# Kernel optimization log

Measured on AMD Instinct MI355X. Metric: run time of the kernel, lower is better.

## Reference

```python
import math
import jax, jax.numpy as jnp
import numpy as np

B, S, D = 8, 1024, 1024
H, DK = 16, 64
NUM_BUCKETS, MAX_DIST = 32, 128
LN_EPS = 1e-6


def _relative_position_bucket(relative_position, num_buckets=NUM_BUCKETS, max_distance=MAX_DIST):
    # bidirectional (encoder) variant of T5 bucketing
    nb = num_buckets // 2
    rel_buckets = (relative_position > 0).astype(jnp.int32) * nb
    rp = jnp.abs(relative_position)
    max_exact = nb // 2
    is_small = rp < max_exact
    rp_large = max_exact + (
        jnp.log(jnp.maximum(rp, 1).astype(jnp.float32) / max_exact)
        / math.log(max_distance / max_exact)
        * (nb - max_exact)
    ).astype(jnp.int32)
    rp_large = jnp.minimum(rp_large, nb - 1)
    return rel_buckets + jnp.where(is_small, rp, rp_large)


def compute_bias(rel_bias, q_len, k_len):
    ctx = jnp.arange(q_len)[:, None]
    mem = jnp.arange(k_len)[None, :]
    buckets = _relative_position_bucket(mem - ctx)        # [q,k]
    values = rel_bias[buckets]                             # [q,k,H]
    return jnp.transpose(values, (2, 0, 1))[None]          # [1,H,q,k]


def switch_layer_norm(x, w, eps=LN_EPS):
    # T5-style: no mean subtraction, no bias
    var = jnp.mean(jnp.square(x.astype(jnp.float32)), axis=-1, keepdims=True)
    return w * (x * jax.lax.rsqrt(var + eps)).astype(x.dtype)


def setup_inputs() -> dict:
    key = jax.random.key(0)
    ks = jax.random.split(key, 6)
    scale = 1.0 / math.sqrt(D)
    return {
        "hidden_states": jax.random.normal(ks[0], (B, S, D), jnp.float32),
        "ln_weight": jnp.ones((D,), jnp.float32),
        "wq": jax.random.normal(ks[1], (D, H * DK), jnp.float32) * scale,
        "wk": jax.random.normal(ks[2], (D, H * DK), jnp.float32) * scale,
        "wv": jax.random.normal(ks[3], (D, H * DK), jnp.float32) * scale,
        "wo": jax.random.normal(ks[4], (H * DK, D), jnp.float32) * scale,
        "rel_bias": jax.random.normal(ks[5], (NUM_BUCKETS, H), jnp.float32),
    }


def reference(hidden_states, ln_weight, wq, wk, wv, wo, rel_bias):
    b, s, d = hidden_states.shape
    normed = switch_layer_norm(hidden_states, ln_weight)
    # projections -> [B,H,S,DK]; T5 applies NO 1/sqrt(dk) scaling
    q = (normed @ wq).reshape(b, s, H, DK).transpose(0, 2, 1, 3)
    k = (normed @ wk).reshape(b, s, H, DK).transpose(0, 2, 1, 3)
    v = (normed @ wv).reshape(b, s, H, DK).transpose(0, 2, 1, 3)
    scores = jnp.einsum("bhqd,bhkd->bhqk", q, k)
    scores = scores + compute_bias(rel_bias, s, s)
    attn = jax.nn.softmax(scores, axis=-1)
    ctx = jnp.einsum("bhqk,bhkd->bhqd", attn, v)
    ctx = ctx.transpose(0, 2, 1, 3).reshape(b, s, H * DK)
    attn_out = ctx @ wo
    return hidden_states + attn_out  # residual of SwitchLayerSelfAttention (dropout=0)
```

## Files before the change

kernel.cpp:

```cpp
#include <hip/hip_runtime.h>

typedef unsigned short u16;
typedef unsigned int u32;
typedef unsigned long long u64;
typedef __attribute__((ext_vector_type(8))) short bf16x8;
typedef __attribute__((ext_vector_type(4))) float f32x4;

__device__ __forceinline__ float bf2f(u16 u) {
  union { u32 i; float f; } c; c.i = ((u32)u) << 16; return c.f;
}
__device__ __forceinline__ u16 f2bf(float f) {
  union { float f; u32 i; } c; c.f = f;
  u32 i = c.i;
  return (u16)((i + 0x7fffu + ((i >> 16) & 1u)) >> 16);
}
__device__ __forceinline__ u32 pkbf(float a, float b) {
  union { float f; u32 i; } ca, cb; ca.f = a; cb.f = b;
  return __builtin_amdgcn_perm(cb.i + 0x8000u, ca.i + 0x8000u, 0x07060302u);
}
__device__ __forceinline__ void async16(const void* g, void* l) {
  __builtin_amdgcn_global_load_lds((const __attribute__((address_space(1))) void*)g,
                                   (__attribute__((address_space(3))) void*)l, 16, 0, 0);
}

__global__ __launch_bounds__(256) void detect_kernel(const u32* __restrict__ X,
                                                     int* __restrict__ flag) {
  __shared__ int part[4];
  const int tid = threadIdx.x, lane = tid & 63, wave = tid >> 6;
  int votes = 0;
  for (int i = tid; i < 4096; i += 256) {
    const u32 u = X[i];
    union { u32 i; float f; } c; c.i = u;
    const float a = fabsf(c.f);
    if (u == 0u || (a > 1e-6f && a < 1e6f)) votes++;
  }
  #pragma unroll
  for (int off = 32; off >= 1; off >>= 1) votes += __shfl_xor(votes, off);
  if (lane == 0) part[wave] = votes;
  __syncthreads();
  if (tid == 0) {
    const int tot = part[0] + part[1] + part[2] + part[3];
    *flag = (tot >= 2048) ? 0 : 1;
  }
}

__global__ __launch_bounds__(256) void prep_rms_kernel(
    const void* __restrict__ W0, const void* __restrict__ W1, const void* __restrict__ W2,
    const void* __restrict__ W3, u16* __restrict__ T0, u16* __restrict__ T1,
    u16* __restrict__ T2, u16* __restrict__ T3, const void* __restrict__ rel_bias,
    float* __restrict__ Tb, const void* __restrict__ X, const void* __restrict__ LnW,
    u16* __restrict__ Normed, const int* __restrict__ flagp) {
  const int f32m = (*flagp == 0);
  const int z = blockIdx.z;
  if (z >= 5) {
    __shared__ float part[4];
    const int tid = threadIdx.x, lane = tid & 63, wave = tid >> 6;
    const size_t row = (size_t)(z - 5) * 256 + blockIdx.y * 16 + blockIdx.x;
    const int c = tid * 4;
    float x0, x1, x2, x3, w0f, w1f, w2f, w3f;
    if (f32m) {
      const float4 xx = *(const float4*)((const float*)X + row * 1024 + c);
      x0 = xx.x; x1 = xx.y; x2 = xx.z; x3 = xx.w;
      const float4 ww = *(const float4*)((const float*)LnW + c);
      w0f = ww.x; w1f = ww.y; w2f = ww.z; w3f = ww.w;
    } else {
      const u32* px = (const u32*)((const u16*)X + row * 1024 + c);
      const u32 a0 = px[0], a1 = px[1];
      x0 = bf2f((u16)a0); x1 = bf2f((u16)(a0 >> 16));
      x2 = bf2f((u16)a1); x3 = bf2f((u16)(a1 >> 16));
      const u32* pw = (const u32*)((const u16*)LnW + c);
      const u32 b0 = pw[0], b1 = pw[1];
      w0f = bf2f((u16)b0); w1f = bf2f((u16)(b0 >> 16));
      w2f = bf2f((u16)b1); w3f = bf2f((u16)(b1 >> 16));
    }
    float ss = x0 * x0 + x1 * x1 + x2 * x2 + x3 * x3;
    #pragma unroll
    for (int off = 32; off >= 1; off >>= 1) ss += __shfl_xor(ss, off);
    if (lane == 0) part[wave] = ss;
    __syncthreads();
    const float tot = part[0] + part[1] + part[2] + part[3];
    const float scale = rsqrtf(tot * (1.0f / 1024.0f) + 1e-6f);
    const u16 o0 = f2bf(x0 * scale * w0f);
    const u16 o1 = f2bf(x1 * scale * w1f);
    const u16 o2 = f2bf(x2 * scale * w2f);
    const u16 o3 = f2bf(x3 * scale * w3f);
    u32* po = (u32*)(Normed + row * 1024 + c);
    po[0] = (u32)o0 | ((u32)o1 << 16);
    po[1] = (u32)o2 | ((u32)o3 << 16);
    return;
  }
  if (z == 4) {
    const int flat = blockIdx.y * 16 + blockIdx.x;
    const int idx = flat * 256 + threadIdx.x;
    if (idx >= 16 * 2047) return;
    const int h = idx / 2047;
    const int d = idx % 2047 - 1023;
    const int rb = (d > 0) ? 16 : 0;
    const int rp = d < 0 ? -d : d;
    int val;
    if (rp < 8) {
      val = rp;
    } else {
      float t = (logf((float)rp * 0.125f) / 2.772588722239781f) * 8.0f;
      val = 8 + (int)t;
      if (val > 15) val = 15;
    }
    const int bi = (rb + val) * 16 + h;
    Tb[idx] = f32m ? ((const float*)rel_bias)[bi] : bf2f(((const u16*)rel_bias)[bi]);
    return;
  }
  const void* W = (z == 0) ? W0 : (z == 1) ? W1 : (z == 2) ? W2 : W3;
  u16* WT = (z == 0) ? T0 : (z == 1) ? T1 : (z == 2) ? T2 : T3;
  __shared__ u16 t[64][65];
  const int tid = threadIdx.x;
  const int tx = tid & 63, ty = tid >> 6;
  const int n0 = blockIdx.x * 64, k0 = blockIdx.y * 64;
  #pragma unroll
  for (int r = ty; r < 64; r += 4) {
    const size_t idx = (size_t)(k0 + r) * 1024 + n0 + tx;
    t[r][tx] = f32m ? f2bf(((const float*)W)[idx]) : ((const u16*)W)[idx];
  }
  __syncthreads();
  #pragma unroll
  for (int r = ty; r < 64; r += 4) WT[(size_t)(n0 + r) * 1024 + k0 + tx] = t[tx][r];
}

template <int S0>
__device__ __forceinline__ void stage3(u16* lds, const u16* __restrict__ A,
                                       const u16* __restrict__ B, int m0, int n0,
                                       int kt, int w, int lane) {
  const int ko8 = ((lane & 7) ^ ((lane >> 3) & 7)) * 8;
  const int rl = lane >> 3;
  #pragma unroll
  for (int s = S0; s < S0 + 3; ++s) {
    const int cw = s * 8 + w;
    const int r = cw * 8 + rl;
    u16* ldst = lds + cw * 512;
    if (s < 4)
      async16(A + (size_t)(m0 + r) * 1024 + kt + ko8, ldst);
    else
      async16(B + (size_t)(n0 + r - 256) * 1024 + kt + ko8, ldst);
  }
}

template <bool SWAP>
__device__ __forceinline__ void gemm256_core(const u16* __restrict__ A,
                                             const u16* __restrict__ WT,
                                             u16 (*buf)[24576], f32x4 (&acc)[4][4],
                                             int m0, int n0, int lane, int w) {
  const int wr = w >> 1, wc = w & 1;
  const int l15 = lane & 15;
  const int ko0 = (((lane >> 4) + 0) ^ (lane & 7)) * 8;
  const int ko1 = (((lane >> 4) + 4) ^ (lane & 7)) * 8;
  const int arow = (wr * 64 + l15) * 64;
  const int brow = 16384 + (wc * 64 + l15) * 64;

  stage3<0>(buf[0], A, WT, m0, n0, 0, w, lane);
  stage3<3>(buf[0], A, WT, m0, n0, 0, w, lane);
  stage3<0>(buf[1], A, WT, m0, n0, 64, w, lane);
  stage3<3>(buf[1], A, WT, m0, n0, 64, w, lane);
  __asm__ volatile("s_waitcnt vmcnt(6)" ::: "memory");
  __builtin_amdgcn_s_barrier();
  __asm__ volatile("" ::: "memory");

  int sl = 0, sn = 2;
  #pragma unroll 1
  for (int t = 0; t < 16; ++t) {
    const u16* bc = buf[sl];
    u16* bn = buf[sn];
    const int kt2 = (t + 2) * 64;
    bf16x8 af[4][2], bfr[2][2];
    #pragma unroll
    for (int i = 0; i < 4; ++i) {
      af[i][0] = *(const bf16x8*)(bc + arow + i * 1024 + ko0);
      af[i][1] = *(const bf16x8*)(bc + arow + i * 1024 + ko1);
    }
    #pragma unroll
    for (int j = 0; j < 2; ++j) {
      bfr[j][0] = *(const bf16x8*)(bc + brow + j * 1024 + ko0);
      bfr[j][1] = *(const bf16x8*)(bc + brow + j * 1024 + ko1);
    }
    if (t < 14) stage3<0>(bn, A, WT, m0, n0, kt2, w, lane);
    __builtin_amdgcn_s_barrier();
    __asm__ volatile("s_waitcnt lgkmcnt(0)" ::: "memory");
    __builtin_amdgcn_s_setprio(1);
    #pragma unroll
    for (int i = 0; i < 4; ++i)
      #pragma unroll
      for (int j = 0; j < 2; ++j) {
        if (SWAP) {
          acc[i][j] = __builtin_amdgcn_mfma_f32_16x16x32_bf16(bfr[j][0], af[i][0], acc[i][j], 0, 0, 0);
          acc[i][j] = __builtin_amdgcn_mfma_f32_16x16x32_bf16(bfr[j][1], af[i][1], acc[i][j], 0, 0, 0);
        } else {
          acc[i][j] = __builtin_amdgcn_mfma_f32_16x16x32_bf16(af[i][0], bfr[j][0], acc[i][j], 0, 0, 0);
          acc[i][j] = __builtin_amdgcn_mfma_f32_16x16x32_bf16(af[i][1], bfr[j][1], acc[i][j], 0, 0, 0);
        }
      }
    __builtin_amdgcn_s_setprio(0);
    __builtin_amdgcn_s_barrier();
    __asm__ volatile("" ::: "memory");
    #pragma unroll
    for (int j = 0; j < 2; ++j) {
      bfr[j][0] = *(const bf16x8*)(bc + brow + (j + 2) * 1024 + ko0);
      bfr[j][1] = *(const bf16x8*)(bc + brow + (j + 2) * 1024 + ko1);
    }
    if (t < 14) stage3<3>(bn, A, WT, m0, n0, kt2, w, lane);
    __builtin_amdgcn_s_barrier();
    __asm__ volatile("s_waitcnt lgkmcnt(0)" ::: "memory");
    __builtin_amdgcn_s_setprio(1);
    #pragma unroll
    for (int i = 0; i < 4; ++i)
      #pragma unroll
      for (int j = 0; j < 2; ++j) {
        if (SWAP) {
          acc[i][j + 2] = __builtin_amdgcn_mfma_f32_16x16x32_bf16(bfr[j][0], af[i][0], acc[i][j + 2], 0, 0, 0);
          acc[i][j + 2] = __builtin_amdgcn_mfma_f32_16x16x32_bf16(bfr[j][1], af[i][1], acc[i][j + 2], 0, 0, 0);
        } else {
          acc[i][j + 2] = __builtin_amdgcn_mfma_f32_16x16x32_bf16(af[i][0], bfr[j][0], acc[i][j + 2], 0, 0, 0);
          acc[i][j + 2] = __builtin_amdgcn_mfma_f32_16x16x32_bf16(af[i][1], bfr[j][1], acc[i][j + 2], 0, 0, 0);
        }
      }
    __builtin_amdgcn_s_setprio(0);
    if (t < 14)
      __asm__ volatile("s_waitcnt vmcnt(6)" ::: "memory");
    else
      __asm__ volatile("s_waitcnt vmcnt(0)" ::: "memory");
    __builtin_amdgcn_s_barrier();
    __asm__ volatile("" ::: "memory");
    sl = (sl == 2) ? 0 : sl + 1;
    sn = (sn == 2) ? 0 : sn + 1;
  }
}

__device__ __forceinline__ void stageK32(u16* lds, const u16* __restrict__ A,
                                         const u16* __restrict__ B, int m0, int n0,
                                         int kt, int w, int lane) {
  const int sp = (lane & 7) ^ ((lane >> 3) & 7);
  const int rl = 2 * (lane >> 3) + (sp >> 2);
  const int ko = (sp & 3) * 8;
  #pragma unroll
  for (int s = 0; s < 3; ++s) {
    const int cw = s * 8 + w;
    u16* ldst = lds + cw * 512;
    if (s < 2)
      async16(A + (size_t)(m0 + cw * 16 + rl) * 1024 + kt + ko, ldst);
    else
      async16(B + (size_t)(n0 + (cw - 16) * 16 + rl) * 1024 + kt + ko, ldst);
  }
}

template <bool SWAP>
__device__ __forceinline__ void gemmK32_core(const u16* __restrict__ A,
                                             const u16* __restrict__ WT,
                                             u16 (*buf)[12288], f32x4 (&acc)[4][4],
                                             int m0, int n0, int lane, int w) {
  const int wr = w >> 1, wc = w & 1;
  const int l15 = lane & 15, quad = lane >> 4;
  const int sw = ((quad + 4 * (lane & 1)) ^ ((l15 >> 1) & 7)) * 8;
  const int abase = (wr * 32 + (l15 >> 1)) * 64 + sw;
  const int bbase = 8192 + (wc * 32 + (l15 >> 1)) * 64 + sw;

  stageK32(buf[0], A, WT, m0, n0, 0, w, lane);
  stageK32(buf[1], A, WT, m0, n0, 32, w, lane);
  __asm__ volatile("s_waitcnt vmcnt(3)" ::: "memory");
  __builtin_amdgcn_s_barrier();
  __asm__ volatile("" ::: "memory");

  int sl = 0, sn = 2;
  #pragma unroll 1
  for (int t = 0; t < 32; ++t) {
    const u16* bc = buf[sl];
    bf16x8 af[4], bfr[4];
    #pragma unroll
    for (int i = 0; i < 4; ++i) af[i] = *(const bf16x8*)(bc + abase + i * 512);
    #pragma unroll
    for (int j = 0; j < 4; ++j) bfr[j] = *(const bf16x8*)(bc + bbase + j * 512);
    if (t < 30) stageK32(buf[sn], A, WT, m0, n0, (t + 2) * 32, w, lane);
    __asm__ volatile("s_waitcnt lgkmcnt(0)" ::: "memory");
    __builtin_amdgcn_s_setprio(1);
    #pragma unroll
    for (int i = 0; i < 4; ++i)
      #pragma unroll
      for (int j = 0; j < 4; ++j) {
        if (SWAP)
          acc[i][j] = __builtin_amdgcn_mfma_f32_16x16x32_bf16(bfr[j], af[i], acc[i][j], 0, 0, 0);
        else
          acc[i][j] = __builtin_amdgcn_mfma_f32_16x16x32_bf16(af[i], bfr[j], acc[i][j], 0, 0, 0);
      }
    __builtin_amdgcn_s_setprio(0);
    if (t < 30)
      __asm__ volatile("s_waitcnt vmcnt(3)" ::: "memory");
    else
      __asm__ volatile("s_waitcnt vmcnt(0)" ::: "memory");
    __builtin_amdgcn_s_barrier();
    __asm__ volatile("" ::: "memory");
    sl = (sl == 2) ? 0 : sl + 1;
    sn = (sn == 2) ? 0 : sn + 1;
  }
}

__global__ __launch_bounds__(512, 4) void qkv_gemm32_kernel(
    const u16* __restrict__ A, const u16* __restrict__ WT,
    u16* __restrict__ Qo, u16* __restrict__ Ko, u16* __restrict__ VTo) {
  __shared__ __align__(16) u16 buf[3][12288];
  const int tid = threadIdx.x, lane = tid & 63, w = tid >> 6;
  const int id = blockIdx.x;
  const int xcd = id & 7;
  const int t0 = id >> 3;
  const int nb = t0 % 24;
  const int mhi = t0 / 24;
  const int m0 = (mhi * 8 + xcd) * 256;
  const int n0 = nb * 128;
  const int z = nb >> 3;

  f32x4 acc[4][4];
  const f32x4 zero = {0.f, 0.f, 0.f, 0.f};
  #pragma unroll
  for (int i = 0; i < 4; ++i)
    #pragma unroll
    for (int j = 0; j < 4; ++j) acc[i][j] = zero;

  const int wr = w >> 1, wc = w & 1;
  const int cq = lane & 15, quad = lane >> 4;
  const int nbase = (n0 & 1023) + wc * 64;

  if (z == 2) {
    gemmK32_core<false>(A, WT, buf, acc, m0, n0, lane, w);
    #pragma unroll
    for (int i = 0; i < 4; ++i) {
      const int s = m0 + wr * 64 + i * 16 + quad * 4;
      const int b = s >> 10, s0 = s & 1023;
      #pragma unroll
      for (int j = 0; j < 4; ++j) {
        const int n = nbase + j * 16 + cq;
        const int hh = n >> 6, dk = n & 63;
        const u64 pk = (u64)f2bf(acc[i][j][0]) | ((u64)f2bf(acc[i][j][1]) << 16) |
                       ((u64)f2bf(acc[i][j][2]) << 32) | ((u64)f2bf(acc[i][j][3]) << 48);
        *(u64*)(VTo + (((size_t)(b * 16 + hh)) * 64 + dk) * 1024 + s0) = pk;
      }
    }
  } else {
    gemmK32_core<true>(A, WT, buf, acc, m0, n0, lane, w);
    u16* Out = (z == 0) ? Qo : Ko;
    #pragma unroll
    for (int i = 0; i < 4; ++i) {
      const int s = m0 + wr * 64 + i * 16 + cq;
      const int b = s >> 10, ss = s & 1023;
      #pragma unroll
      for (int j = 0; j < 4; ++j) {
        const int n = nbase + j * 16 + quad * 4;
        const int hh = n >> 6, dk = n & 63;
        const u64 pk = (u64)f2bf(acc[i][j][0]) | ((u64)f2bf(acc[i][j][1]) << 16) |
                       ((u64)f2bf(acc[i][j][2]) << 32) | ((u64)f2bf(acc[i][j][3]) << 48);
        *(u64*)(Out + (((size_t)(b * 16 + hh)) * 1024 + ss) * 64 + dk) = pk;
      }
    }
  }
}

__global__ __launch_bounds__(512, 2) void out_gemm256_kernel(
    const u16* __restrict__ A, const u16* __restrict__ BT, const void* __restrict__ Res,
    void* __restrict__ Out, const int* __restrict__ flagp) {
  const int f32m = (*flagp == 0);
  __shared__ __align__(16) u16 buf[3][24576];
  const int tid = threadIdx.x, lane = tid & 63, w = tid >> 6;
  const int id = blockIdx.x;
  const int xcd = id & 7;
  const int t0 = id >> 3;
  const int nb = t0 & 7;
  const int mhi = t0 >> 3;
  const int m0 = (mhi * 8 + xcd) * 256;
  const int n0 = nb * 128;

  f32x4 acc[4][4];
  const f32x4 zero = {0.f, 0.f, 0.f, 0.f};
  #pragma unroll
  for (int i = 0; i < 4; ++i)
    #pragma unroll
    for (int j = 0; j < 4; ++j) acc[i][j] = zero;

  gemm256_core<true>(A, BT, buf, acc, m0, n0, lane, w);

  const int wr = w >> 1, wc = w & 1;
  const int cq = lane & 15, quad = lane >> 4;
  #pragma unroll
  for (int i = 0; i < 4; ++i) {
    const int s = m0 + wr * 64 + i * 16 + cq;
    #pragma unroll
    for (int j = 0; j < 4; ++j) {
      const int n = n0 + wc * 64 + j * 16 + quad * 4;
      const size_t idx = (size_t)s * 1024 + n;
      if (f32m) {
        const float4 rr = *(const float4*)((const float*)Res + idx);
        float4 oo;
        oo.x = rr.x + acc[i][j][0]; oo.y = rr.y + acc[i][j][1];
        oo.z = rr.z + acc[i][j][2]; oo.w = rr.w + acc[i][j][3];
        *(float4*)((float*)Out + idx) = oo;
      } else {
        const u64 rr = *(const u64*)((const u16*)Res + idx);
        const u64 pk =
            (u64)f2bf(bf2f((u16)rr) + acc[i][j][0]) |
            ((u64)f2bf(bf2f((u16)(rr >> 16)) + acc[i][j][1]) << 16) |
            ((u64)f2bf(bf2f((u16)(rr >> 32)) + acc[i][j][2]) << 32) |
            ((u64)f2bf(bf2f((u16)(rr >> 48)) + acc[i][j][3]) << 48);
        *(u64*)((u16*)Out + idx) = pk;
      }
    }
  }
}

__global__ __launch_bounds__(512, 4) void attn_kernel(
    const u16* __restrict__ Q, const u16* __restrict__ K, const u16* __restrict__ VT,
    const float* __restrict__ Tb, u16* __restrict__ ctx) {
  __shared__ __align__(16) u16 Ks[3][4096];
  __shared__ __align__(16) u16 Vs[2][4096];
  __shared__ __align__(16) u16 Ps[8][2048];
  __shared__ __align__(16) float Tbs[1280];

  const int tid = threadIdx.x, lane = tid & 63, w = tid >> 6;
  const int c = lane & 15, quad = lane >> 4;
  const int id = blockIdx.x;
  const int bh = id & 127, qc = id >> 7;
  const int b = bh >> 4, h = bh & 15;
  const int q0 = qc * 256;
  const int qw = q0 + w * 32;
  const u16* Kg = K + (size_t)bh * 1024 * 64;
  const u16* Vg = VT + (size_t)bh * 64 * 1024;
  const float* Th = Tb + h * 2047;
  u16* PsW = &Ps[w][0];

  for (int i = tid; i < 1280; i += 512) Tbs[i] = Th[768 - q0 + i];

  bf16x8 qf[2][2];
  {
    const u16* Qg = Q + ((size_t)bh * 1024 + qw) * 64;
    #pragma unroll
    for (int nt = 0; nt < 2; ++nt)
      #pragma unroll
      for (int half = 0; half < 2; ++half)
        qf[nt][half] = *(const bf16x8*)(Qg + (size_t)(nt * 16 + c) * 64 + half * 32 + quad * 8);
  }

  f32x4 oacc[4][2];
  const f32x4 zero = {0.f, 0.f, 0.f, 0.f};
  #pragma unroll
  for (int i = 0; i < 4; ++i)
    #pragma unroll
    for (int j = 0; j < 2; ++j) oacc[i][j] = zero;
  float rsum[2] = {0.f, 0.f};

  const u16* Ksrc = Kg + (size_t)((w >> 1) * 16 + c) * 64 + (w & 1) * 32 + quad * 8;
  const u16* Vsrc = Vg + (size_t)((w >> 1) * 16 + c) * 1024 + (w & 1) * 32 + quad * 8;

  async16(Vsrc, &Vs[0][w * 512]);
  async16(Ksrc, &Ks[0][w * 512]);
  async16(Ksrc + (size_t)64 * 64, &Ks[1][w * 512]);
  __asm__ volatile("s_waitcnt lgkmcnt(0)" ::: "memory");

  int sl = 0, sn = 2;
  #pragma unroll 1
  for (int kt = 0; kt < 16; ++kt) {
    const int k0 = kt * 64;
    const u16* Kc = &Ks[sl][0];
    const u16* Vc = &Vs[kt & 1][0];
    if (kt < 15)
      __asm__ volatile("s_waitcnt vmcnt(1)" ::: "memory");
    else
      __asm__ volatile("s_waitcnt vmcnt(0)" ::: "memory");
    __builtin_amdgcn_s_barrier();
    __asm__ volatile("" ::: "memory");
    if (kt < 15) async16(Vsrc + (kt + 1) * 64, &Vs[(kt + 1) & 1][w * 512]);
    if (kt < 14) async16(Ksrc + (size_t)((kt + 2) * 64) * 64, &Ks[sn][w * 512]);
    f32x4 sc[4][2];
    const int jb = k0 + quad * 4 - c + 255 - 32 * w;
    #pragma unroll
    for (int mt = 0; mt < 4; ++mt)
      #pragma unroll
      for (int nt = 0; nt < 2; ++nt) {
        const float* tp = Tbs + jb + mt * 16 - nt * 16;
        sc[mt][nt][0] = tp[0]; sc[mt][nt][1] = tp[1]; sc[mt][nt][2] = tp[2]; sc[mt][nt][3] = tp[3];
      }
    __builtin_amdgcn_s_setprio(1);
    #pragma unroll
    for (int mt = 0; mt < 4; ++mt) {
      const bf16x8 kf0 = *(const bf16x8*)(Kc + (mt * 2 + 0) * 512 + lane * 8);
      const bf16x8 kf1 = *(const bf16x8*)(Kc + (mt * 2 + 1) * 512 + lane * 8);
      #pragma unroll
      for (int nt = 0; nt < 2; ++nt) {
        sc[mt][nt] = __builtin_amdgcn_mfma_f32_16x16x32_bf16(kf0, qf[nt][0], sc[mt][nt], 0, 0, 0);
        sc[mt][nt] = __builtin_amdgcn_mfma_f32_16x16x32_bf16(kf1, qf[nt][1], sc[mt][nt], 0, 0, 0);
      }
    }
    __builtin_amdgcn_s_setprio(0);
    #pragma unroll
    for (int mt = 0; mt < 4; ++mt)
      #pragma unroll
      for (int nt = 0; nt < 2; ++nt) {
        const float p0 = __expf(sc[mt][nt][0]), p1 = __expf(sc[mt][nt][1]);
        const float p2 = __expf(sc[mt][nt][2]), p3 = __expf(sc[mt][nt][3]);
        rsum[nt] += (p0 + p1) + (p2 + p3);
        const u32 lo = pkbf(p0, p1), hi = pkbf(p2, p3);
        const u64 pk = (u64)lo | ((u64)hi << 32);
        const int ch = (mt * 2 + (quad >> 1)) ^ (c & 7);
        *(u64*)(PsW + (nt * 16 + c) * 64 + ch * 8 + (quad & 1) * 4) = pk;
      }
    __asm__ volatile("s_waitcnt lgkmcnt(0)" ::: "memory");
    bf16x8 pf[2][2];
    #pragma unroll
    for (int nt = 0; nt < 2; ++nt)
      #pragma unroll
      for (int kk = 0; kk < 2; ++kk) {
        const int ch = (kk * 4 + quad) ^ (c & 7);
        pf[nt][kk] = *(const bf16x8*)(PsW + (nt * 16 + c) * 64 + ch * 8);
      }
    __builtin_amdgcn_s_setprio(1);
    #pragma unroll
    for (int dt = 0; dt < 4; ++dt) {
      const bf16x8 vf0 = *(const bf16x8*)(Vc + (dt * 2 + 0) * 512 + lane * 8);
      const bf16x8 vf1 = *(const bf16x8*)(Vc + (dt * 2 + 1) * 512 + lane * 8);
      #pragma unroll
      for (int nt = 0; nt < 2; ++nt) {
        oacc[dt][nt] = __builtin_amdgcn_mfma_f32_16x16x32_bf16(vf0, pf[nt][0], oacc[dt][nt], 0, 0, 0);
        oacc[dt][nt] = __builtin_amdgcn_mfma_f32_16x16x32_bf16(vf1, pf[nt][1], oacc[dt][nt], 0, 0, 0);
      }
    }
    __builtin_amdgcn_s_setprio(0);
    sl = (sl == 2) ? 0 : sl + 1;
    sn = (sn == 2) ? 0 : sn + 1;
  }

  #pragma unroll
  for (int nt = 0; nt < 2; ++nt) {
    rsum[nt] += __shfl_xor(rsum[nt], 16);
    rsum[nt] += __shfl_xor(rsum[nt], 32);
  }

  #pragma unroll
  for (int nt = 0; nt < 2; ++nt) {
    const float inv = 1.0f / rsum[nt];
    const int q = qw + nt * 16 + c;
    #pragma unroll
    for (int dt = 0; dt < 4; ++dt) {
      const u64 pk = (u64)f2bf(oacc[dt][nt][0] * inv) | ((u64)f2bf(oacc[dt][nt][1] * inv) << 16) |
                     ((u64)f2bf(oacc[dt][nt][2] * inv) << 32) | ((u64)f2bf(oacc[dt][nt][3] * inv) << 48);
      *(u64*)(ctx + (((size_t)b * 1024 + q) * 16 + h) * 64 + dt * 16 + quad * 4) = pk;
    }
  }
}

extern "C" void kernel_launch(void* const* d_in, const int* in_sizes, int n_in,
                              void* d_out, int out_size, void* d_ws, size_t ws_size,
                              hipStream_t stream) {
  const void* hidden = d_in[0];
  const void* lnw = d_in[1];
  const void* wq = d_in[2];
  const void* wk = d_in[3];
  const void* wv = d_in[4];
  const void* wo = d_in[5];
  const void* relb = d_in[6];
  char* ws = (char*)d_ws;

  u16* normed = (u16*)(ws);
  u16* Qb = (u16*)(ws + ((size_t)16 << 20));
  u16* Kb = (u16*)(ws + ((size_t)32 << 20));
  u16* VTb = (u16*)(ws + ((size_t)48 << 20));
  u16* wtq = (u16*)(ws + ((size_t)64 << 20));
  u16* wtk = (u16*)(ws + ((size_t)64 << 20) + (2 << 20));
  u16* wtv = (u16*)(ws + ((size_t)64 << 20) + (4 << 20));
  u16* wto = (u16*)(ws + ((size_t)64 << 20) + (6 << 20));
  float* Tb = (float*)(ws + ((size_t)64 << 20) + (8 << 20));
  int* flag = (int*)(ws + ((size_t)64 << 20) + (9 << 20));

  dim3 b256(256);
  detect_kernel<<<dim3(1), b256, 0, stream>>>((const u32*)hidden, flag);
  prep_rms_kernel<<<dim3(16, 16, 37), b256, 0, stream>>>(wq, wk, wv, wo, wtq, wtk, wtv,
                                                         wto, relb, Tb, hidden, lnw,
                                                         normed, flag);
  qkv_gemm32_kernel<<<dim3(768), dim3(512), 0, stream>>>(normed, wtq, Qb, Kb, VTb);
  attn_kernel<<<dim3(512), dim3(512), 0, stream>>>(Qb, Kb, VTb, Tb, normed);
  out_gemm256_kernel<<<dim3(256), dim3(512), 0, stream>>>(normed, wto, hidden, d_out, flag);
}
```

Baseline: 244.7 us.

## Fold dtype detection into kernels and switch output GEMM to K32 core

Removes the separate single-block detect kernel launch and its flag buffer. Each block of the prep and output-projection kernels now recomputes the input-dtype vote itself. The output projection also moves from the 256-deep-K pipelined core to the K32 core used by the QKV GEMM, with half the LDS and a launch bound of 4 blocks per CU for better occupancy. The cost is redundant 16KB reads plus a block barrier in every one of the roughly nine thousand prep blocks and in every output block.

```diff
diff --git a/kernel.cpp b/kernel.cpp
--- a/kernel.cpp
+++ b/kernel.cpp
@@ -23,12 +23,12 @@
                                    (__attribute__((address_space(3))) void*)l, 16, 0, 0);
 }
 
-__global__ __launch_bounds__(256) void detect_kernel(const u32* __restrict__ X,
-                                                     int* __restrict__ flag) {
-  __shared__ int part[4];
-  const int tid = threadIdx.x, lane = tid & 63, wave = tid >> 6;
+template <int NT>
+__device__ __forceinline__ int detect_f32(const u32* __restrict__ X, int* part,
+                                          int tid, int lane, int wave) {
   int votes = 0;
-  for (int i = tid; i < 4096; i += 256) {
+  #pragma unroll
+  for (int i = tid; i < 4096; i += NT) {
     const u32 u = X[i];
     union { u32 i; float f; } c; c.i = u;
     const float a = fabsf(c.f);
@@ -38,10 +38,10 @@
   for (int off = 32; off >= 1; off >>= 1) votes += __shfl_xor(votes, off);
   if (lane == 0) part[wave] = votes;
   __syncthreads();
-  if (tid == 0) {
-    const int tot = part[0] + part[1] + part[2] + part[3];
-    *flag = (tot >= 2048) ? 0 : 1;
-  }
+  int tot = 0;
+  #pragma unroll
+  for (int i = 0; i < NT / 64; ++i) tot += part[i];
+  return (tot >= 2048) ? 1 : 0;
 }
 
 __global__ __launch_bounds__(256) void prep_rms_kernel(
@@ -49,8 +49,10 @@
     const void* __restrict__ W3, u16* __restrict__ T0, u16* __restrict__ T1,
     u16* __restrict__ T2, u16* __restrict__ T3, const void* __restrict__ rel_bias,
     float* __restrict__ Tb, const void* __restrict__ X, const void* __restrict__ LnW,
-    u16* __restrict__ Normed, const int* __restrict__ flagp) {
-  const int f32m = (*flagp == 0);
+    u16* __restrict__ Normed) {
+  __shared__ int dpart[4];
+  const int tid0 = threadIdx.x;
+  const int f32m = detect_f32<256>((const u32*)X, dpart, tid0, tid0 & 63, tid0 >> 6);
   const int z = blockIdx.z;
   if (z >= 5) {
     __shared__ float part[4];
@@ -125,113 +127,6 @@
   for (int r = ty; r < 64; r += 4) WT[(size_t)(n0 + r) * 1024 + k0 + tx] = t[tx][r];
 }
 
-template <int S0>
-__device__ __forceinline__ void stage3(u16* lds, const u16* __restrict__ A,
-                                       const u16* __restrict__ B, int m0, int n0,
-                                       int kt, int w, int lane) {
-  const int ko8 = ((lane & 7) ^ ((lane >> 3) & 7)) * 8;
-  const int rl = lane >> 3;
-  #pragma unroll
-  for (int s = S0; s < S0 + 3; ++s) {
-    const int cw = s * 8 + w;
-    const int r = cw * 8 + rl;
-    u16* ldst = lds + cw * 512;
-    if (s < 4)
-      async16(A + (size_t)(m0 + r) * 1024 + kt + ko8, ldst);
-    else
-      async16(B + (size_t)(n0 + r - 256) * 1024 + kt + ko8, ldst);
-  }
-}
-
-template <bool SWAP>
-__device__ __forceinline__ void gemm256_core(const u16* __restrict__ A,
-                                             const u16* __restrict__ WT,
-                                             u16 (*buf)[24576], f32x4 (&acc)[4][4],
-                                             int m0, int n0, int lane, int w) {
-  const int wr = w >> 1, wc = w & 1;
-  const int l15 = lane & 15;
-  const int ko0 = (((lane >> 4) + 0) ^ (lane & 7)) * 8;
-  const int ko1 = (((lane >> 4) + 4) ^ (lane & 7)) * 8;
-  const int arow = (wr * 64 + l15) * 64;
-  const int brow = 16384 + (wc * 64 + l15) * 64;
-
-  stage3<0>(buf[0], A, WT, m0, n0, 0, w, lane);
-  stage3<3>(buf[0], A, WT, m0, n0, 0, w, lane);
-  stage3<0>(buf[1], A, WT, m0, n0, 64, w, lane);
-  stage3<3>(buf[1], A, WT, m0, n0, 64, w, lane);
-  __asm__ volatile("s_waitcnt vmcnt(6)" ::: "memory");
-  __builtin_amdgcn_s_barrier();
-  __asm__ volatile("" ::: "memory");
-
-  int sl = 0, sn = 2;
-  #pragma unroll 1
-  for (int t = 0; t < 16; ++t) {
-    const u16* bc = buf[sl];
-    u16* bn = buf[sn];
-    const int kt2 = (t + 2) * 64;
-    bf16x8 af[4][2], bfr[2][2];
-    #pragma unroll
-    for (int i = 0; i < 4; ++i) {
-      af[i][0] = *(const bf16x8*)(bc + arow + i * 1024 + ko0);
-      af[i][1] = *(const bf16x8*)(bc + arow + i * 1024 + ko1);
-    }
-    #pragma unroll
-    for (int j = 0; j < 2; ++j) {
-      bfr[j][0] = *(const bf16x8*)(bc + brow + j * 1024 + ko0);
-      bfr[j][1] = *(const bf16x8*)(bc + brow + j * 1024 + ko1);
-    }
-    if (t < 14) stage3<0>(bn, A, WT, m0, n0, kt2, w, lane);
-    __builtin_amdgcn_s_barrier();
-    __asm__ volatile("s_waitcnt lgkmcnt(0)" ::: "memory");
-    __builtin_amdgcn_s_setprio(1);
-    #pragma unroll
-    for (int i = 0; i < 4; ++i)
-      #pragma unroll
-      for (int j = 0; j < 2; ++j) {
-        if (SWAP) {
-          acc[i][j] = __builtin_amdgcn_mfma_f32_16x16x32_bf16(bfr[j][0], af[i][0], acc[i][j], 0, 0, 0);
-          acc[i][j] = __builtin_amdgcn_mfma_f32_16x16x32_bf16(bfr[j][1], af[i][1], acc[i][j], 0, 0, 0);
-        } else {
-          acc[i][j] = __builtin_amdgcn_mfma_f32_16x16x32_bf16(af[i][0], bfr[j][0], acc[i][j], 0, 0, 0);
-          acc[i][j] = __builtin_amdgcn_mfma_f32_16x16x32_bf16(af[i][1], bfr[j][1], acc[i][j], 0, 0, 0);
-        }
-      }
-    __builtin_amdgcn_s_setprio(0);
-    __builtin_amdgcn_s_barrier();
-    __asm__ volatile("" ::: "memory");
-    #pragma unroll
-    for (int j = 0; j < 2; ++j) {
-      bfr[j][0] = *(const bf16x8*)(bc + brow + (j + 2) * 1024 + ko0);
-      bfr[j][1] = *(const bf16x8*)(bc + brow + (j + 2) * 1024 + ko1);
-    }
-    if (t < 14) stage3<3>(bn, A, WT, m0, n0, kt2, w, lane);
-    __builtin_amdgcn_s_barrier();
-    __asm__ volatile("s_waitcnt lgkmcnt(0)" ::: "memory");
-    __builtin_amdgcn_s_setprio(1);
-    #pragma unroll
-    for (int i = 0; i < 4; ++i)
-      #pragma unroll
-      for (int j = 0; j < 2; ++j) {
-        if (SWAP) {
-          acc[i][j + 2] = __builtin_amdgcn_mfma_f32_16x16x32_bf16(bfr[j][0], af[i][0], acc[i][j + 2], 0, 0, 0);
-          acc[i][j + 2] = __builtin_amdgcn_mfma_f32_16x16x32_bf16(bfr[j][1], af[i][1], acc[i][j + 2], 0, 0, 0);
-        } else {
-          acc[i][j + 2] = __builtin_amdgcn_mfma_f32_16x16x32_bf16(af[i][0], bfr[j][0], acc[i][j + 2], 0, 0, 0);
-          acc[i][j + 2] = __builtin_amdgcn_mfma_f32_16x16x32_bf16(af[i][1], bfr[j][1], acc[i][j + 2], 0, 0, 0);
-        }
-      }
-    __builtin_amdgcn_s_setprio(0);
-    if (t < 14)
-      __asm__ volatile("s_waitcnt vmcnt(6)" ::: "memory");
-    else
-      __asm__ volatile("s_waitcnt vmcnt(0)" ::: "memory");
-    __builtin_amdgcn_s_barrier();
-    __asm__ volatile("" ::: "memory");
-    sl = (sl == 2) ? 0 : sl + 1;
-    sn = (sn == 2) ? 0 : sn + 1;
-  }
-}
-
 __device__ __forceinline__ void stageK32(u16* lds, const u16* __restrict__ A,
                                          const u16* __restrict__ B, int m0, int n0,
                                          int kt, int w, int lane) {
@@ -358,12 +253,13 @@
   }
 }
 
-__global__ __launch_bounds__(512, 2) void out_gemm256_kernel(
+__global__ __launch_bounds__(512, 4) void out_gemm32_kernel(
     const u16* __restrict__ A, const u16* __restrict__ BT, const void* __restrict__ Res,
-    void* __restrict__ Out, const int* __restrict__ flagp) {
-  const int f32m = (*flagp == 0);
-  __shared__ __align__(16) u16 buf[3][24576];
+    void* __restrict__ Out) {
+  __shared__ __align__(16) u16 buf[3][12288];
+  __shared__ int dpart[8];
   const int tid = threadIdx.x, lane = tid & 63, w = tid >> 6;
+  const int f32m = detect_f32<512>((const u32*)Res, dpart, tid, lane, w);
   const int id = blockIdx.x;
   const int xcd = id & 7;
   const int t0 = id >> 3;
@@ -379,7 +275,7 @@
     #pragma unroll
     for (int j = 0; j < 4; ++j) acc[i][j] = zero;
 
-  gemm256_core<true>(A, BT, buf, acc, m0, n0, lane, w);
+  gemmK32_core<true>(A, BT, buf, acc, m0, n0, lane, w);
 
   const int wr = w >> 1, wc = w & 1;
   const int cq = lane & 15, quad = lane >> 4;
@@ -569,14 +465,12 @@
   u16* wtv = (u16*)(ws + ((size_t)64 << 20) + (4 << 20));
   u16* wto = (u16*)(ws + ((size_t)64 << 20) + (6 << 20));
   float* Tb = (float*)(ws + ((size_t)64 << 20) + (8 << 20));
-  int* flag = (int*)(ws + ((size_t)64 << 20) + (9 << 20));
 
   dim3 b256(256);
-  detect_kernel<<<dim3(1), b256, 0, stream>>>((const u32*)hidden, flag);
   prep_rms_kernel<<<dim3(16, 16, 37), b256, 0, stream>>>(wq, wk, wv, wo, wtq, wtk, wtv,
                                                          wto, relb, Tb, hidden, lnw,
-                                                         normed, flag);
+                                                         normed);
   qkv_gemm32_kernel<<<dim3(768), dim3(512), 0, stream>>>(normed, wtq, Qb, Kb, VTb);
   attn_kernel<<<dim3(512), dim3(512), 0, stream>>>(Qb, Kb, VTb, Tb, normed);
-  out_gemm256_kernel<<<dim3(256), dim3(512), 0, stream>>>(normed, wto, hidden, d_out, flag);
-}
+  out_gemm32_kernel<<<dim3(256), dim3(512), 0, stream>>>(normed, wto, hidden, d_out);
+}
```

After: 257.9 us. 1.05x slower.
